# Performance work log

Hardware: AMD Instinct MI355X
Metric: run time of the kernel (lower is better)

## Reference

```python
import jax, jax.numpy as jnp
import numpy as np

E = 1024  # embedding_dim
D = 1024  # output_dim

def setup_inputs() -> dict:
    key = jax.random.key(0)
    k_x, k_q, k_k, k_v = jax.random.split(key, 4)
    embeddings = jax.random.normal(k_x, (4, 2048, E), dtype=jnp.float32)
    scale = 1.0 / np.sqrt(E)
    Wq = jax.random.normal(k_q, (E, D), dtype=jnp.float32) * scale
    Wk = jax.random.normal(k_k, (E, D), dtype=jnp.float32) * scale
    Wv = jax.random.normal(k_v, (E, D), dtype=jnp.float32) * scale
    return {"embeddings": embeddings, "Wq": Wq, "Wk": Wk, "Wv": Wv}

def reference(embeddings, Wq, Wk, Wv):
    # QKV projections (no bias, qkv_bias=False)
    q = jnp.einsum('bse,ed->bsd', embeddings, Wq)
    k = jnp.einsum('bse,ed->bsd', embeddings, Wk)
    v = jnp.einsum('bse,ed->bsd', embeddings, Wv)
    n = embeddings.shape[1]
    scores = jnp.einsum('bqd,bkd->bqk', q, k)  # [B, S, S]
    causal = jnp.tril(jnp.ones((n, n), dtype=bool))  # mask upper triangle (diag=1)
    scores = jnp.where(causal, scores, -jnp.inf)
    scale = jnp.asarray(k.shape[-1], scores.dtype) ** 0.5
    weights = jax.nn.softmax(scores / scale, axis=-1)
    # dropout p=0.0 -> identity
    context = jnp.einsum('bqk,bkd->bqd', weights, v)
    return context
```

## Files before the change

### kernel.cpp

```cpp
#include <hip/hip_runtime.h>
#include <hip/hip_fp16.h>

typedef unsigned short u16;
typedef __attribute__((ext_vector_type(8))) short short8;
typedef __attribute__((ext_vector_type(4))) float f32x4;
typedef __attribute__((ext_vector_type(4))) unsigned short u16x4;
typedef __attribute__((ext_vector_type(4))) float float4v;

__device__ __forceinline__ u16 f2bf(float f) {
  union { float f; unsigned u; } v; v.f = f;
  unsigned r = v.u + 0x7FFFu + ((v.u >> 16) & 1u);
  return (u16)(r >> 16);
}

__device__ __forceinline__ u16 f2h(float f) {
  __half h = __float2half(f);
  return *reinterpret_cast<u16*>(&h);
}

__device__ __forceinline__ float h2f(u16 b) {
  __half_raw hr; hr.x = b;
  return __half2float(__half(hr));
}

__device__ __forceinline__ void gload16(const void* g, void* l) {
  __builtin_amdgcn_global_load_lds(
      (const __attribute__((address_space(1))) unsigned int*)g,
      (__attribute__((address_space(3))) unsigned int*)l, 16, 0, 0);
}

__global__ __launch_bounds__(256) void kconvW(const float* __restrict__ Wq,
                                              const float* __restrict__ Wk,
                                              const float* __restrict__ Wv,
                                              u16* __restrict__ Wqb,
                                              u16* __restrict__ Wkb,
                                              u16* __restrict__ Wvt) {
  __shared__ float tile[32][33];
  const int bx = blockIdx.x, t = threadIdx.x;
  if (bx < 2048) {
    const float* W = bx < 1024 ? Wq : Wk;
    u16* O = bx < 1024 ? Wqb : Wkb;
    size_t i = ((size_t)(bx & 1023) * 256 + t) * 4;
    float4v v = *(const float4v*)(W + i);
    u16x4 o;
    o.x = f2bf(v.x); o.y = f2bf(v.y); o.z = f2bf(v.z); o.w = f2bf(v.w);
    *(u16x4*)(O + i) = o;
  } else {
    const int rem = bx - 2048;
    const int n0 = (rem & 31) * 32, k0 = (rem >> 5) * 32;
    const int tx = t & 31, ty = t >> 5;
#pragma unroll
    for (int r = 0; r < 32; r += 8)
      tile[ty + r][tx] = Wv[(size_t)(k0 + ty + r) * 1024 + n0 + tx];
    __syncthreads();
#pragma unroll
    for (int r = 0; r < 32; r += 8)
      Wvt[(size_t)(n0 + ty + r) * 1024 + k0 + tx] = f2bf(tile[tx][ty + r]);
  }
}

__device__ __forceinline__ void stage64(const u16* __restrict__ pan, int ld,
                                        int k0, u16* dst, int t) {
  const int rb = t >> 3;
  const int sw = ((t & 7) ^ (rb & 7)) * 8;
  const int ds = (t & 7) * 8;
#pragma unroll
  for (int j = 0; j < 4; ++j) {
    const int row = j * 32 + rb;
    gload16(pan + (size_t)row * ld + k0 + sw, dst + row * 64 + ds);
  }
}

__device__ __forceinline__ void gemm64(const u16* __restrict__ A,
                                       const u16* __restrict__ B,
                                       int lda, int ldb,
                                       int rowBase, int colBase, int kIters,
                                       u16* As, u16* Bs, f32x4 acc[4][4]) {
  const int t = threadIdx.x;
  const int wid = t >> 6, lane = t & 63;
  const int wm = wid >> 1, wn = wid & 1;
  const int l15 = lane & 15;
  const int sw = l15 & 7;
  const int sl = lane >> 4;
  const int s0 = ((sl    ) ^ sw) * 8;
  const int s1 = ((sl + 4) ^ sw) * 8;
  const u16* ga = A + (size_t)rowBase * lda;
  const u16* gb = B + (size_t)colBase * ldb;

  for (int kt = 0; kt < kIters; ++kt) {
    const int k0 = kt * 64;
    stage64(ga, lda, k0, As, t);
    stage64(gb, ldb, k0, Bs, t);
    __syncthreads();
#pragma unroll
    for (int h = 0; h < 2; ++h) {
      const int so = h ? s1 : s0;
      short8 a[4], b[4];
#pragma unroll
      for (int mi = 0; mi < 4; mi++)
        a[mi] = *(const short8*)(As + (wm * 64 + mi * 16 + l15) * 64 + so);
#pragma unroll
      for (int ni = 0; ni < 4; ni++)
        b[ni] = *(const short8*)(Bs + (wn * 64 + ni * 16 + l15) * 64 + so);
#pragma unroll
      for (int mi = 0; mi < 4; mi++)
#pragma unroll
        for (int ni = 0; ni < 4; ni++)
          acc[mi][ni] = __builtin_amdgcn_mfma_f32_16x16x32_bf16(
              a[mi], b[ni], acc[mi][ni], 0, 0, 0);
    }
    __syncthreads();
  }
}

__global__ __launch_bounds__(256) void kconvX(const float* __restrict__ X,
                                              const u16* __restrict__ Wqb,
                                              const u16* __restrict__ Wkb,
                                              u16* __restrict__ Xb,
                                              u16* __restrict__ Mt) {
  __shared__ __align__(16) u16 As[128 * 64];
  __shared__ __align__(16) u16 Bs[128 * 64];
  const int bx = blockIdx.x, t = threadIdx.x;
  if (bx < 64) {
    const f32x4 z4 = {0.f, 0.f, 0.f, 0.f};
    f32x4 acc[4][4];
#pragma unroll
    for (int i = 0; i < 4; i++)
#pragma unroll
      for (int j = 0; j < 4; j++) acc[i][j] = z4;

    const int rowBase = (bx >> 3) * 128, colBase = (bx & 7) * 128;
    gemm64(Wkb, Wqb, 1024, 1024, rowBase, colBase, 16, As, Bs, acc);

    const int wid = t >> 6, lane = t & 63;
    const int wm = wid >> 1, wn = wid & 1;
    const int r0 = rowBase + wm * 64 + ((lane >> 4) * 4);
    const int c0 = colBase + wn * 64 + (lane & 15);
#pragma unroll
    for (int mi = 0; mi < 4; mi++) {
      int r = r0 + mi * 16;
#pragma unroll
      for (int ni = 0; ni < 4; ni++) {
        int c = c0 + ni * 16;
#pragma unroll
        for (int j = 0; j < 4; j++)
          Mt[(size_t)(r + j) * 1024 + c] = f2bf(acc[mi][ni][j] * 0.03125f);
      }
    }
  } else {
    const int l = bx - 64;
    size_t i = ((size_t)l * 256 + t) * 4;
    float4v v = *(const float4v*)(X + i);
    u16x4 o;
    o.x = f2bf(v.x); o.y = f2bf(v.y); o.z = f2bf(v.z); o.w = f2bf(v.w);
    *(u16x4*)(Xb + i) = o;
  }
}

__global__ __launch_bounds__(256, 4) void kqkv(const u16* __restrict__ Xb,
                                               const u16* __restrict__ Mt,
                                               const u16* __restrict__ Wvt,
                                               u16* __restrict__ Qb,
                                               u16* __restrict__ Vt) {
  __shared__ __align__(16) u16 As[128 * 64];
  __shared__ __align__(16) u16 Bs[128 * 64];
  const f32x4 z4 = {0.f, 0.f, 0.f, 0.f};
  f32x4 acc[4][4];
#pragma unroll
  for (int i = 0; i < 4; i++)
#pragma unroll
    for (int j = 0; j < 4; j++) acc[i][j] = z4;

  const int l = blockIdx.x;
  const int xcd = l & 7, idx = l >> 3;
  const int cz = idx >> 3, rloc = idx & 7;
  const int rowTile = xcd * 8 + rloc;
  const int z = cz >> 3, colTile = cz & 7;

  const int rowBase = rowTile * 128, colBase = colTile * 128;
  const u16* Bt = z ? Wvt : Mt;
  gemm64(Xb, Bt, 1024, 1024, rowBase, colBase, 16, As, Bs, acc);

  const int t = threadIdx.x, wid = t >> 6, lane = t & 63;
  const int wm = wid >> 1, wn = wid & 1;
  const int r0 = rowBase + wm * 64 + ((lane >> 4) * 4);
  const int c0 = colBase + wn * 64 + (lane & 15);
  if (z == 0) {
#pragma unroll
    for (int mi = 0; mi < 4; mi++) {
      int r = r0 + mi * 16;
#pragma unroll
      for (int ni = 0; ni < 4; ni++) {
        int c = c0 + ni * 16;
#pragma unroll
        for (int j = 0; j < 4; j++)
          Qb[(size_t)(r + j) * 1024 + c] = f2bf(acc[mi][ni][j]);
      }
    }
  } else {
#pragma unroll
    for (int mi = 0; mi < 4; mi++) {
      int s0r = r0 + mi * 16;
      int bb = s0r >> 11, sl = s0r & 2047;
#pragma unroll
      for (int ni = 0; ni < 4; ni++) {
        int d = c0 + ni * 16;
        u16x4 pk;
        pk.x = f2bf(acc[mi][ni][0]);
        pk.y = f2bf(acc[mi][ni][1]);
        pk.z = f2bf(acc[mi][ni][2]);
        pk.w = f2bf(acc[mi][ni][3]);
        *(u16x4*)(Vt + ((size_t)bb * 1024 + d) * 2048 + sl) = pk;
      }
    }
  }
}

__global__ __launch_bounds__(256, 3) void kscores(const u16* __restrict__ Q,
                                                  const u16* __restrict__ Xb,
                                                  u16* __restrict__ Sch) {
  const int x = blockIdx.x, b = blockIdx.y;
  const int xcd = x & 7, idx = x >> 3;
  const int tid = xcd * 17 + idx;
  int tr = (int)((sqrtf(8.f * tid + 1.f) - 1.f) * 0.5f);
  while ((tr + 1) * (tr + 2) / 2 <= tid) ++tr;
  while (tr * (tr + 1) / 2 > tid) --tr;
  const int tc = tid - tr * (tr + 1) / 2;

  __shared__ __align__(16) u16 As[128 * 64];
  __shared__ __align__(16) u16 Bs[128 * 64];
  const f32x4 z4 = {0.f, 0.f, 0.f, 0.f};
  f32x4 acc[4][4];
#pragma unroll
  for (int i = 0; i < 4; i++)
#pragma unroll
    for (int j = 0; j < 4; j++) acc[i][j] = z4;

  const u16* Qp = Q + (size_t)b * 2048 * 1024;
  const u16* Kp = Xb + (size_t)b * 2048 * 1024;
  gemm64(Qp, Kp, 1024, 1024, tr * 128, tc * 128, 16, As, Bs, acc);

  u16* S = Sch + (size_t)b * 2048 * 2048;
  const int t = threadIdx.x, wid = t >> 6, lane = t & 63;
  const int wm = wid >> 1, wn = wid & 1;
  const int r0 = tr * 128 + wm * 64 + ((lane >> 4) * 4);
  const int c0 = tc * 128 + wn * 64 + (lane & 15);
#pragma unroll
  for (int mi = 0; mi < 4; mi++) {
    int r = r0 + mi * 16;
#pragma unroll
    for (int ni = 0; ni < 4; ni++) {
      int c = c0 + ni * 16;
#pragma unroll
      for (int j = 0; j < 4; j++)
        S[(size_t)(r + j) * 2048 + c] = f2h(acc[mi][ni][j]);
    }
  }
}

__global__ __launch_bounds__(256) void ksoftmax(const u16* __restrict__ Sch,
                                                u16* __restrict__ P) {
  const int i = blockIdx.x, b = blockIdx.y;
  const int t = threadIdx.x, lane = t & 63, wid = t >> 6;
  const int nceil = ((i >> 7) + 1) << 7;
  __shared__ float red[4];

  const size_t rowoff = ((size_t)b * 2048 + i) * 2048 + t * 8;
  const int base = t * 8;
  short8 raw = {0, 0, 0, 0, 0, 0, 0, 0};
  if (base < nceil) raw = *(const short8*)(Sch + rowoff);
  float v[8];
#pragma unroll
  for (int k = 0; k < 8; ++k)
    v[k] = (base + k <= i) ? h2f((u16)raw[k]) : -3.0e38f;

  float lm = v[0];
#pragma unroll
  for (int k = 1; k < 8; ++k) lm = fmaxf(lm, v[k]);
#pragma unroll
  for (int o = 32; o > 0; o >>= 1) lm = fmaxf(lm, __shfl_down(lm, o));
  if (lane == 0) red[wid] = lm;
  __syncthreads();
  const float m = fmaxf(fmaxf(red[0], red[1]), fmaxf(red[2], red[3]));
  __syncthreads();

  float e[8], ls = 0.f;
#pragma unroll
  for (int k = 0; k < 8; ++k) {
    e[k] = __expf(fmaxf(v[k] - m, -88.f));
    ls += e[k];
  }
#pragma unroll
  for (int o = 32; o > 0; o >>= 1) ls += __shfl_down(ls, o);
  if (lane == 0) red[wid] = ls;
  __syncthreads();
  const float inv = 1.f / (red[0] + red[1] + red[2] + red[3]);

  if (base < nceil) {
    short8 out;
#pragma unroll
    for (int k = 0; k < 8; ++k) out[k] = (short)f2bf(e[k] * inv);
    *(short8*)(P + rowoff) = out;
  }
}

__global__ __launch_bounds__(256, 3) void kpv(const u16* __restrict__ P,
                                              const u16* __restrict__ Vt,
                                              float* __restrict__ Out) {
  const int x = blockIdx.x, b = blockIdx.y;
  const int xcd = x & 7, idx = x >> 3;
  const int tr = ((idx & 1) ^ (b >> 1)) ? (15 - xcd) : xcd;
  const int col = idx >> 1;

  __shared__ __align__(16) u16 As[128 * 64];
  __shared__ __align__(16) u16 Bs[128 * 64];
  const f32x4 z4 = {0.f, 0.f, 0.f, 0.f};
  f32x4 acc[4][4];
#pragma unroll
  for (int i = 0; i < 4; i++)
#pragma unroll
    for (int j = 0; j < 4; j++) acc[i][j] = z4;

  const u16* Pp = P + (size_t)b * 2048 * 2048;
  const u16* Vp = Vt + (size_t)b * 1024 * 2048;
  gemm64(Pp, Vp, 2048, 2048, tr * 128, col * 128, (tr + 1) * 2, As, Bs, acc);

  float* Ob = Out + (size_t)b * 2048 * 1024;
  const int t = threadIdx.x, wid = t >> 6, lane = t & 63;
  const int wm = wid >> 1, wn = wid & 1;
  const int r0 = tr * 128 + wm * 64 + ((lane >> 4) * 4);
  const int c0 = col * 128 + wn * 64 + (lane & 15);
#pragma unroll
  for (int mi = 0; mi < 4; mi++) {
    int r = r0 + mi * 16;
#pragma unroll
    for (int ni = 0; ni < 4; ni++) {
      int c = c0 + ni * 16;
#pragma unroll
      for (int j = 0; j < 4; j++)
        Ob[(size_t)(r + j) * 1024 + c] = acc[mi][ni][j];
    }
  }
}

extern "C" void kernel_launch(void* const* d_in, const int* in_sizes, int n_in,
                              void* d_out, int out_size, void* d_ws,
                              size_t ws_size, hipStream_t stream) {
  const float* X = (const float*)d_in[0];
  const float* Wq = (const float*)d_in[1];
  const float* Wk = (const float*)d_in[2];
  const float* Wv = (const float*)d_in[3];
  float* Out = (float*)d_out;

  char* ws = (char*)d_ws;
  u16* Xb  = (u16*)(ws);
  u16* Wvt = (u16*)(ws + 16777216);
  u16* Mt  = (u16*)(ws + 18874368);
  u16* Qb  = (u16*)(ws + 20971520);
  u16* Vt  = (u16*)(ws + 37748736);
  u16* Sch = (u16*)(ws + 54525952);
  u16* P   = (u16*)(ws + 88080384);
  u16* Wqb = (u16*)(ws + 121634816);
  u16* Wkb = (u16*)(ws + 123731968);

  kconvW<<<3072, 256, 0, stream>>>(Wq, Wk, Wv, Wqb, Wkb, Wvt);
  kconvX<<<8256, 256, 0, stream>>>(X, Wqb, Wkb, Xb, Mt);
  kqkv<<<1024, 256, 0, stream>>>(Xb, Mt, Wvt, Qb, Vt);
  kscores<<<dim3(136, 4), 256, 0, stream>>>(Qb, Xb, Sch);
  ksoftmax<<<dim3(2048, 4), 256, 0, stream>>>(Sch, P);
  kpv<<<dim3(128, 4), 256, 0, stream>>>(P, Vt, Out);
}
```

Before: 139.9 us.

## Split-K the causal PV GEMM with atomic accumulation into pre-zeroed output

The P·V kernel now splits each row tile's causal K range into chunks of at most 8 iterations, so 40 work items per column cover the 16 row tiles with balanced lengths, and the grid grows from 128 to 320 blocks per batch. Partial results are combined with float atomic adds into the output. The output is zeroed by extra blocks appended to the weight-conversion kernel. This targets the load imbalance and low block count of the triangular PV GEMM, at the cost of atomic traffic on fp32 output, extra zeroing writes and nondeterministic summation order.

```diff
diff --git a/kernel.cpp b/kernel.cpp
--- a/kernel.cpp
+++ b/kernel.cpp
@@ -34,7 +34,8 @@
                                               const float* __restrict__ Wv,
                                               u16* __restrict__ Wqb,
                                               u16* __restrict__ Wkb,
-                                              u16* __restrict__ Wvt) {
+                                              u16* __restrict__ Wvt,
+                                              float* __restrict__ Out) {
   __shared__ float tile[32][33];
   const int bx = blockIdx.x, t = threadIdx.x;
   if (bx < 2048) {
@@ -45,7 +46,7 @@
     u16x4 o;
     o.x = f2bf(v.x); o.y = f2bf(v.y); o.z = f2bf(v.z); o.w = f2bf(v.w);
     *(u16x4*)(O + i) = o;
-  } else {
+  } else if (bx < 3072) {
     const int rem = bx - 2048;
     const int n0 = (rem & 31) * 32, k0 = (rem >> 5) * 32;
     const int tx = t & 31, ty = t >> 5;
@@ -56,6 +57,12 @@
 #pragma unroll
     for (int r = 0; r < 32; r += 8)
       Wvt[(size_t)(n0 + ty + r) * 1024 + k0 + tx] = f2bf(tile[tx][ty + r]);
+  } else {
+    const int l = bx - 3072;
+    const float4v z = {0.f, 0.f, 0.f, 0.f};
+    float* p = Out + (size_t)l * 8192 + t * 4;
+#pragma unroll
+    for (int j = 0; j < 8; ++j) *(float4v*)(p + j * 1024) = z;
   }
 }
 
@@ -74,7 +81,8 @@
 __device__ __forceinline__ void gemm64(const u16* __restrict__ A,
                                        const u16* __restrict__ B,
                                        int lda, int ldb,
-                                       int rowBase, int colBase, int kIters,
+                                       int rowBase, int colBase,
+                                       int kFirst, int kCount,
                                        u16* As, u16* Bs, f32x4 acc[4][4]) {
   const int t = threadIdx.x;
   const int wid = t >> 6, lane = t & 63;
@@ -87,7 +95,7 @@
   const u16* ga = A + (size_t)rowBase * lda;
   const u16* gb = B + (size_t)colBase * ldb;
 
-  for (int kt = 0; kt < kIters; ++kt) {
+  for (int kt = kFirst; kt < kFirst + kCount; ++kt) {
     const int k0 = kt * 64;
     stage64(ga, lda, k0, As, t);
     stage64(gb, ldb, k0, Bs, t);
@@ -130,7 +138,7 @@
       for (int j = 0; j < 4; j++) acc[i][j] = z4;
 
     const int rowBase = (bx >> 3) * 128, colBase = (bx & 7) * 128;
-    gemm64(Wkb, Wqb, 1024, 1024, rowBase, colBase, 16, As, Bs, acc);
+    gemm64(Wkb, Wqb, 1024, 1024, rowBase, colBase, 0, 16, As, Bs, acc);
 
     const int wid = t >> 6, lane = t & 63;
     const int wm = wid >> 1, wn = wid & 1;
@@ -179,7 +187,7 @@
 
   const int rowBase = rowTile * 128, colBase = colTile * 128;
   const u16* Bt = z ? Wvt : Mt;
-  gemm64(Xb, Bt, 1024, 1024, rowBase, colBase, 16, As, Bs, acc);
+  gemm64(Xb, Bt, 1024, 1024, rowBase, colBase, 0, 16, As, Bs, acc);
 
   const int t = threadIdx.x, wid = t >> 6, lane = t & 63;
   const int wm = wid >> 1, wn = wid & 1;
@@ -238,7 +246,7 @@
 
   const u16* Qp = Q + (size_t)b * 2048 * 1024;
   const u16* Kp = Xb + (size_t)b * 2048 * 1024;
-  gemm64(Qp, Kp, 1024, 1024, tr * 128, tc * 128, 16, As, Bs, acc);
+  gemm64(Qp, Kp, 1024, 1024, tr * 128, tc * 128, 0, 16, As, Bs, acc);
 
   u16* S = Sch + (size_t)b * 2048 * 2048;
   const int t = threadIdx.x, wid = t >> 6, lane = t & 63;
@@ -307,10 +315,17 @@
 __global__ __launch_bounds__(256, 3) void kpv(const u16* __restrict__ P,
                                               const u16* __restrict__ Vt,
                                               float* __restrict__ Out) {
-  const int x = blockIdx.x, b = blockIdx.y;
-  const int xcd = x & 7, idx = x >> 3;
-  const int tr = ((idx & 1) ^ (b >> 1)) ? (15 - xcd) : xcd;
-  const int col = idx >> 1;
+  const int c = blockIdx.x, b = blockIdx.y;
+  const int col = c / 40;
+  const int r = c % 40;
+  int tr, q;
+  if (r < 4)       { tr = r;                q = 0; }
+  else if (r < 12) { tr = 4 + (r - 4) / 2;  q = (r - 4) % 2; }
+  else if (r < 24) { tr = 8 + (r - 12) / 3; q = (r - 12) % 3; }
+  else             { tr = 12 + (r - 24) / 4; q = (r - 24) % 4; }
+  const int ktTotal = (tr + 1) * 2;
+  const int kFirst = q * 8;
+  const int kCount = min(8, ktTotal - kFirst);
 
   __shared__ __align__(16) u16 As[128 * 64];
   __shared__ __align__(16) u16 Bs[128 * 64];
@@ -323,7 +338,7 @@
 
   const u16* Pp = P + (size_t)b * 2048 * 2048;
   const u16* Vp = Vt + (size_t)b * 1024 * 2048;
-  gemm64(Pp, Vp, 2048, 2048, tr * 128, col * 128, (tr + 1) * 2, As, Bs, acc);
+  gemm64(Pp, Vp, 2048, 2048, tr * 128, col * 128, kFirst, kCount, As, Bs, acc);
 
   float* Ob = Out + (size_t)b * 2048 * 1024;
   const int t = threadIdx.x, wid = t >> 6, lane = t & 63;
@@ -332,13 +347,13 @@
   const int c0 = col * 128 + wn * 64 + (lane & 15);
 #pragma unroll
   for (int mi = 0; mi < 4; mi++) {
-    int r = r0 + mi * 16;
+    int rr = r0 + mi * 16;
 #pragma unroll
     for (int ni = 0; ni < 4; ni++) {
-      int c = c0 + ni * 16;
+      int cc = c0 + ni * 16;
 #pragma unroll
       for (int j = 0; j < 4; j++)
-        Ob[(size_t)(r + j) * 1024 + c] = acc[mi][ni][j];
+        unsafeAtomicAdd(&Ob[(size_t)(rr + j) * 1024 + cc], acc[mi][ni][j]);
     }
   }
 }
@@ -363,10 +378,10 @@
   u16* Wqb = (u16*)(ws + 121634816);
   u16* Wkb = (u16*)(ws + 123731968);
 
-  kconvW<<<3072, 256, 0, stream>>>(Wq, Wk, Wv, Wqb, Wkb, Wvt);
+  kconvW<<<4096, 256, 0, stream>>>(Wq, Wk, Wv, Wqb, Wkb, Wvt, Out);
   kconvX<<<8256, 256, 0, stream>>>(X, Wqb, Wkb, Xb, Mt);
   kqkv<<<1024, 256, 0, stream>>>(Xb, Mt, Wvt, Qb, Vt);
   kscores<<<dim3(136, 4), 256, 0, stream>>>(Qb, Xb, Sch);
   ksoftmax<<<dim3(2048, 4), 256, 0, stream>>>(Sch, P);
-  kpv<<<dim3(128, 4), 256, 0, stream>>>(P, Vt, Out);
-}
+  kpv<<<dim3(320, 4), 256, 0, stream>>>(P, Vt, Out);
+}
```

New measurement: 178.9 us. +27.8%, slower.
